# Performance work log

Hardware: AMD Instinct MI355X
Metric: run time of the kernel (lower is better)

The kernel has to match this reference:

```python
import jax, jax.numpy as jnp
import numpy as np

B, S, I, H, E, F, K = 512, 512, 128, 128, 8, 20, 2


def setup_inputs() -> dict:
    key = jax.random.key(0)
    ks = jax.random.split(key, 12)
    u = lambda k, shape, a: jax.random.uniform(k, shape, jnp.float32, -a, a)
    bound_h = 1.0 / np.sqrt(H)
    bound_f = 1.0 / np.sqrt(F)
    return {
        "x": jax.random.normal(ks[0], (B, S, I), jnp.float32),
        "w_gate": jax.random.normal(ks[1], (I, E), jnp.float32),
        "W_ih": u(ks[2], (E, H, I), 0.1),
        "W_hh": u(ks[3], (E, H, H), 0.1),
        "b_ih": u(ks[4], (E, H), bound_h),
        "b_hh": u(ks[5], (E, H), bound_h),
        "fc1_w": u(ks[6], (E, F, H), bound_h),
        "fc1_b": u(ks[7], (E, F), bound_h),
        "fc2_w": u(ks[8], (E, 1, F), bound_f),
        "fc2_b": u(ks[9], (E, 1), bound_f),
    }


def _cv_squared(v):
    v = v.astype(jnp.float32)
    return jnp.var(v, ddof=1) / (jnp.mean(v) ** 2 + 1e-10)


def reference(x, w_gate, W_ih, W_hh, b_ih, b_hh, fc1_w, fc1_b, fc2_w, fc2_b):
    loss_coef = 0.01
    b, s, i = x.shape
    e = w_gate.shape[1]
    # --- top-k gating (noisy_gating=False path) ---
    x_mean = x.mean(axis=1)                       # [B, I]
    logits = x_mean @ w_gate                      # [B, E]
    m = min(K + 1, e)
    top_vals, top_idx = jax.lax.top_k(logits, m)
    topk_gates = jax.nn.softmax(top_vals[:, :K], axis=1)
    gates = jnp.zeros_like(logits).at[jnp.arange(b)[:, None], top_idx[:, :K]].set(topk_gates)
    importance = gates.sum(0)
    load = (gates > 0).sum(0).astype(jnp.float32)
    loss = (_cv_squared(importance) + _cv_squared(load)) * loss_coef
    # --- experts: batched tanh-RNN over all experts (gates zero out unselected) ---
    h0 = jnp.zeros((e, b, W_hh.shape[1]), x.dtype)
    xs = jnp.swapaxes(x, 0, 1)                    # [S, B, I]
    def step(h, xt):
        h = jnp.tanh(jnp.einsum('bi,ehi->ebh', xt, W_ih) + b_ih[:, None, :]
                     + jnp.einsum('ebh,egh->ebg', h, W_hh) + b_hh[:, None, :])
        return h, None
    hT, _ = jax.lax.scan(step, h0, xs)            # [E, B, H] last hidden state
    z = jnp.tanh(jnp.einsum('ebh,efh->ebf', hT, fc1_w) + fc1_b[:, None, :])
    out = jnp.einsum('ebf,eof->ebo', z, fc2_w) + fc2_b[:, None, :]  # [E, B, 1]
    # --- weighted combine: y[b] = sum_e gates[b,e] * expert_e(x[b]) ---
    y = jnp.einsum('be,ebo->bo', gates, out)      # [B, 1]
    return y, loss
```

## Files before the change

### kernel.cpp

```cpp
#include <hip/hip_runtime.h>
#include <math.h>

#define B_SZ 512
#define S_SZ 512
#define E_NUM 8
#define F_DIM 20
#define BM 16
#define MAXBLK 71

typedef __attribute__((ext_vector_type(8))) _Float16 f16x8;
typedef __attribute__((ext_vector_type(4))) float f32x4;
#define MFMAH(a, b, c) __builtin_amdgcn_mfma_f32_16x16x32_f16(a, b, c, 0, 0, 0)

__device__ __forceinline__ unsigned pk16(float a, float b) {
  _Float16 ha = (_Float16)a, hb = (_Float16)b;
  unsigned short ua = __builtin_bit_cast(unsigned short, ha);
  unsigned short ub = __builtin_bit_cast(unsigned short, hb);
  return (unsigned)ua | ((unsigned)ub << 16);
}
__device__ __forceinline__ float ftanh(float x) {
  float e = __expf(x + x);
  float r;
  asm("v_rcp_f32 %0, %1" : "=v"(r) : "v"(e + 1.0f));
  return fmaf(-2.0f, r, 1.0f);
}

#define BAR() do {                                        \
  asm volatile("s_waitcnt lgkmcnt(0)" ::: "memory");      \
  __builtin_amdgcn_s_barrier();                           \
  asm volatile("" ::: "memory");                          \
} while (0)

__global__ __launch_bounds__(256) void k_wsplit16(
    const float* __restrict__ W, _Float16* __restrict__ Wh,
    _Float16* __restrict__ Wl) {
  int idx = (blockIdx.x * 256 + threadIdx.x) * 8;
  float4 a = *(const float4*)(W + idx);
  float4 b = *(const float4*)(W + idx + 4);
  float v[8] = {a.x, a.y, a.z, a.w, b.x, b.y, b.z, b.w};
  f16x8 h, l;
#pragma unroll
  for (int j = 0; j < 8; j++) {
    _Float16 hh = (_Float16)v[j];
    h[j] = hh;
    l[j] = (_Float16)((v[j] - (float)hh) * 1024.0f);
  }
  *(f16x8*)(Wh + idx) = h;
  *(f16x8*)(Wl + idx) = l;
}

__global__ __launch_bounds__(512) void k_mean_logits(
    const float* __restrict__ x, const float* __restrict__ w_gate,
    float* __restrict__ logits) {
  __shared__ float sm[512];
  __shared__ float xm[128];
  int b = blockIdx.x;
  int t = threadIdx.x;
  int i = t & 127, s0 = t >> 7;
  const float* xb = x + (size_t)b * (S_SZ * 128);
  float acc = 0.f;
  for (int s = s0; s < S_SZ; s += 4) acc += xb[s * 128 + i];
  sm[t] = acc;
  __syncthreads();
  if (t < 128)
    xm[t] = (sm[t] + sm[t + 128] + sm[t + 256] + sm[t + 384]) * (1.0f / 512.0f);
  __syncthreads();
  if (t < E_NUM) {
    float acc2 = 0.f;
    for (int ii = 0; ii < 128; ii++) acc2 += xm[ii] * w_gate[ii * E_NUM + t];
    logits[b * E_NUM + t] = acc2;
  }
}

__global__ __launch_bounds__(512) void k_gate(
    const float* __restrict__ logits, float* __restrict__ sel_g,
    int* __restrict__ pair_b, int* __restrict__ pair_of,
    int* __restrict__ blk_e, int* __restrict__ blk_p0,
    int* __restrict__ blk_nr, int* __restrict__ nblk,
    float* __restrict__ loss_out) {
  __shared__ float gmat[512][8];
  __shared__ int cnt[8], base[8], pos[8];
  __shared__ float imps[8];
  int t = threadIdx.x;
  if (t < 8) { cnt[t] = 0; pos[t] = 0; }
  float lv[8];
#pragma unroll
  for (int e = 0; e < 8; e++) {
    lv[e] = logits[t * 8 + e];
    gmat[t][e] = 0.f;
  }
  __syncthreads();
  float v0 = -INFINITY, v1 = -INFINITY;
  int i0 = 0, i1 = 0;
#pragma unroll
  for (int e = 0; e < 8; e++) {
    float v = lv[e];
    if (v > v0) { v1 = v0; i1 = i0; v0 = v; i0 = e; }
    else if (v > v1) { v1 = v; i1 = e; }
  }
  float ex = expf(v1 - v0);
  float inv = 1.0f / (1.0f + ex);
  float g0 = inv, g1 = ex * inv;
  gmat[t][i0] = g0;
  gmat[t][i1] = g1;
  atomicAdd(&cnt[i0], 1);
  atomicAdd(&cnt[i1], 1);
  sel_g[t * 2] = g0;
  sel_g[t * 2 + 1] = g1;
  __syncthreads();
  if (t == 0) {
    int o = 0;
    for (int e = 0; e < 8; e++) { base[e] = o; o += cnt[e]; }
    int nb = 0;
    for (int e = 0; e < 8; e++)
      for (int off = 0; off < cnt[e]; off += BM) {
        blk_e[nb] = e;
        blk_p0[nb] = base[e] + off;
        blk_nr[nb] = min(BM, cnt[e] - off);
        nb++;
      }
    *nblk = nb;
  }
  if (t < 8) {
    float s = 0.f;
    for (int bb = 0; bb < 512; bb++) s += gmat[bb][t];
    imps[t] = s;
  }
  __syncthreads();
  {
    int r = atomicAdd(&pos[i0], 1);
    int p = base[i0] + r;
    pair_b[p] = t;
    pair_of[t * 2] = p;
  }
  {
    int r = atomicAdd(&pos[i1], 1);
    int p = base[i1] + r;
    pair_b[p] = t;
    pair_of[t * 2 + 1] = p;
  }
  if (t == 0) {
    float mi = 0.f, ml = 0.f;
#pragma unroll
    for (int e = 0; e < 8; e++) { mi += imps[e]; ml += (float)cnt[e]; }
    mi *= 0.125f; ml *= 0.125f;
    float vi = 0.f, vl = 0.f;
#pragma unroll
    for (int e = 0; e < 8; e++) {
      float di = imps[e] - mi; vi += di * di;
      float dl = (float)cnt[e] - ml; vl += dl * dl;
    }
    vi *= (1.0f / 7.0f);
    vl *= (1.0f / 7.0f);
    loss_out[0] = 0.01f * (vi / (mi * mi + 1e-10f) + vl / (ml * ml + 1e-10f));
  }
}

__global__ __launch_bounds__(512, 2) void k_moe(
    const float* __restrict__ x, const _Float16* __restrict__ Wih_h,
    const _Float16* __restrict__ Wih_l, const float* __restrict__ W_hh,
    const float* __restrict__ b_ih, const float* __restrict__ b_hh,
    const float* __restrict__ fc1_w, const float* __restrict__ fc1_b,
    const float* __restrict__ fc2_w, const float* __restrict__ fc2_b,
    const int* __restrict__ pair_b, const int* __restrict__ blk_e,
    const int* __restrict__ blk_p0, const int* __restrict__ blk_nr,
    const int* __restrict__ nblk, float* __restrict__ outp) {
  __shared__ unsigned short sX[4][2048];
  __shared__ float sP[2][2048];
  __shared__ unsigned short sH[2][2048];
  __shared__ float sZ[BM * F_DIM];

  int blk = blockIdx.x;
  if (blk >= *nblk) return;
  int e = blk_e[blk], p0 = blk_p0[blk], nr = blk_nr[blk];
  int tid = threadIdx.x;
  int lane = tid & 63, g = lane >> 4, ln = lane & 15;
  int wv = tid >> 6;

  char* sxb = (char*)&sX[0][0];
  char* spb = (char*)&sP[0][0];
  char* shb = (char*)&sH[0][0];

  ((unsigned int*)shb)[tid] = 0;
  ((unsigned int*)shb)[tid + 512] = 0;

  int swz = (ln & 7) << 4;
  int rdoff[4];
#pragma unroll
  for (int ks = 0; ks < 4; ks++) rdoff[ks] = (ln * 256 + ks * 64 + g * 16) ^ swz;

  const f32x4 Z4 = {0.f, 0.f, 0.f, 0.f};

  if (wv < 4) {
    int w = wv;
    f16x8 wih_h[2][4], wih_l[2][4];
#pragma unroll
    for (int m = 0; m < 2; m++) {
      int row = (2 * w + m) * 16 + ln;
      const _Float16* bh = Wih_h + (size_t)e * 16384 + row * 128 + g * 8;
      const _Float16* bl = Wih_l + (size_t)e * 16384 + row * 128 + g * 8;
#pragma unroll
      for (int ks = 0; ks < 4; ks++) {
        wih_h[m][ks] = *(const f16x8*)(bh + ks * 32);
        wih_l[m][ks] = *(const f16x8*)(bl + ks * 32);
      }
    }
    f32x4 biasv[2];
#pragma unroll
    for (int m = 0; m < 2; m++)
#pragma unroll
      for (int r = 0; r < 4; r++) {
        int h = (2 * w + m) * 16 + g * 4 + r;
        biasv[m][r] = b_ih[e * 128 + h] + b_hh[e * 128 + h];
      }
    int pwoff[2];
#pragma unroll
    for (int m = 0; m < 2; m++)
      pwoff[m] = (2 * w + m) * 1024 + g * 256 + ln * 16;

    int srow = 4 * w + (lane >> 4);
    int k0 = (lane & 15) * 8;
    int sb = pair_b[p0 + (srow < nr ? srow : 0)];
    const char* xsrc = (const char*)x + (size_t)sb * (S_SZ * 512) + k0 * 4;
    int stoff = (srow * 256 + k0 * 2) ^ ((srow & 7) << 4);

    float4 xa0, xa1, xb0, xb1;

#define LDX(B0, B1, STEP)                                                    \
  do {                                                                       \
    B0 = *(const float4*)(xsrc + (size_t)(STEP) * 512);                      \
    B1 = *(const float4*)(xsrc + (size_t)(STEP) * 512 + 16);                 \
  } while (0)

#define STG(WS, B0, B1)                                                      \
  do {                                                                       \
    float v[8] = {B0.x, B0.y, B0.z, B0.w, B1.x, B1.y, B1.z, B1.w};           \
    f16x8 hx;                                                                \
    _Pragma("unroll") for (int j = 0; j < 8; j++) hx[j] = (_Float16)v[j];    \
    *(f16x8*)(sxb + ((WS) << 12) + stoff) = hx;                              \
  } while (0)

#define PRD(XS, PS)                                                          \
  do {                                                                       \
    f16x8 Xf[4];                                                             \
    _Pragma("unroll") for (int ks = 0; ks < 4; ks++)                         \
        Xf[ks] = *(const f16x8*)(sxb + ((XS) << 12) + rdoff[ks]);            \
    _Pragma("unroll") for (int m = 0; m < 2; m++) {                          \
      f32x4 pA = biasv[m];                                                   \
      _Pragma("unroll") for (int ks = 0; ks < 4; ks++)                       \
          pA = MFMAH(wih_h[m][ks], Xf[ks], pA);                              \
      f32x4 pB = Z4;                                                         \
      _Pragma("unroll") for (int ks = 0; ks < 4; ks++)                       \
          pB = MFMAH(wih_l[m][ks], Xf[ks], pB);                              \
      _Pragma("unroll") for (int r = 0; r < 4; r++)                          \
          pA[r] = fmaf(pB[r], 0.0009765625f, pA[r]);                         \
      *(f32x4*)(spb + ((PS) << 13) + pwoff[m]) = pA;                         \
    }                                                                        \
  } while (0)

    LDX(xa0, xa1, 0);
    LDX(xb0, xb1, 1);
    STG(0, xa0, xa1);
    STG(1, xb0, xb1);
    LDX(xa0, xa1, 2);
    LDX(xb0, xb1, 3);
    BAR();
    PRD(0, 0);
    STG(2, xa0, xa1);
    LDX(xa0, xa1, 4);
    BAR();

#pragma unroll 1
    for (int r4 = 0; r4 < 504; r4 += 4) {
      PRD(1, 1); STG(3, xb0, xb1); LDX(xb0, xb1, r4 + 5); BAR();
      PRD(2, 0); STG(0, xa0, xa1); LDX(xa0, xa1, r4 + 6); BAR();
      PRD(3, 1); STG(1, xb0, xb1); LDX(xb0, xb1, r4 + 7); BAR();
      PRD(0, 0); STG(2, xa0, xa1); LDX(xa0, xa1, r4 + 8); BAR();
    }
    PRD(1, 1); STG(3, xb0, xb1); LDX(xb0, xb1, 509); BAR();
    PRD(2, 0); STG(0, xa0, xa1); LDX(xa0, xa1, 510); BAR();
    PRD(3, 1); STG(1, xb0, xb1); LDX(xb0, xb1, 511); BAR();
    PRD(0, 0); STG(2, xa0, xa1); BAR();
    PRD(1, 1); STG(3, xb0, xb1); BAR();
    PRD(2, 0); BAR();
    PRD(3, 1); BAR();
    BAR();
#undef PRD
#undef STG
#undef LDX
  } else {
    int w2 = wv - 4;
    f16x8 wh[2][4], wl[2][4];
#pragma unroll
    for (int m = 0; m < 2; m++) {
      int row = (2 * w2 + m) * 16 + ln;
      const float* bh = W_hh + (size_t)e * 16384 + row * 128 + g * 8;
#pragma unroll
      for (int ks = 0; ks < 4; ks++) {
        float4 a = *(const float4*)(bh + ks * 32);
        float4 b = *(const float4*)(bh + ks * 32 + 4);
        float v[8] = {a.x, a.y, a.z, a.w, b.x, b.y, b.z, b.w};
        f16x8 h, l;
#pragma unroll
        for (int j = 0; j < 8; j++) {
          _Float16 hh = (_Float16)v[j];
          h[j] = hh;
          l[j] = (_Float16)((v[j] - (float)hh) * 1024.0f);
        }
        wh[m][ks] = h;
        wl[m][ks] = l;
      }
    }
    int proff[2], wroff[2];
#pragma unroll
    for (int m = 0; m < 2; m++) {
      proff[m] = (2 * w2 + m) * 1024 + g * 256 + ln * 16;
      wroff[m] = (ln * 256 + (2 * w2 + m) * 32 + g * 8) ^ swz;
    }

#define CRD(RS)                                                              \
  do {                                                                       \
    f16x8 Hf[4];                                                             \
    _Pragma("unroll") for (int ks = 0; ks < 4; ks++)                         \
        Hf[ks] = *(const f16x8*)(shb + (RS) * 4096 + rdoff[ks]);             \
    _Pragma("unroll") for (int m = 0; m < 2; m++) {                          \
      f32x4 preA = *(const f32x4*)(spb + ((RS) << 13) + proff[m]);           \
      _Pragma("unroll") for (int ks = 0; ks < 4; ks++)                       \
          preA = MFMAH(wh[m][ks], Hf[ks], preA);                             \
      f32x4 preB = Z4;                                                       \
      _Pragma("unroll") for (int ks = 0; ks < 4; ks++)                       \
          preB = MFMAH(wl[m][ks], Hf[ks], preB);                             \
      _Pragma("unroll") for (int r = 0; r < 4; r++)                          \
          preA[r] = fmaf(preB[r], 0.0009765625f, preA[r]);                   \
      float t0 = ftanh(preA[0]), t1 = ftanh(preA[1]);                        \
      float t2 = ftanh(preA[2]), t3 = ftanh(preA[3]);                        \
      uint2 hv = {pk16(t0, t1), pk16(t2, t3)};                               \
      *(uint2*)(shb + ((RS) ^ 1) * 4096 + wroff[m]) = hv;                    \
    }                                                                        \
  } while (0)

    BAR();
    BAR();
#pragma unroll 1
    for (int it = 0; it < 128; it++) {
      CRD(0); BAR();
      CRD(1); BAR();
      CRD(0); BAR();
      CRD(1); BAR();
    }
#undef CRD
  }

  {
    int p = tid >> 5, q = tid & 31;
    if (q < F_DIM) {
      float acc = fc1_b[e * F_DIM + q];
      const float* w1 = fc1_w + (size_t)e * (F_DIM * 128) + q * 128;
      for (int k = 0; k < 128; k++) {
        int off = (p * 256 + k * 2) ^ ((p & 7) << 4);
        float h = (float)(*(const _Float16*)(shb + off));
        acc = fmaf(h, w1[k], acc);
      }
      sZ[p * F_DIM + q] = ftanh(acc);
    }
  }
  __syncthreads();
  if (tid < BM) {
    float acc = fc2_b[e];
#pragma unroll
    for (int f = 0; f < F_DIM; f++)
      acc += sZ[tid * F_DIM + f] * fc2_w[e * F_DIM + f];
    if (tid < nr) outp[p0 + tid] = acc;
  }
}

__global__ void k_combine(const float* __restrict__ sel_g,
                          const int* __restrict__ pair_of,
                          const float* __restrict__ outp,
                          float* __restrict__ y) {
  int b = blockIdx.x * blockDim.x + threadIdx.x;
  if (b < B_SZ)
    y[b] = sel_g[2 * b] * outp[pair_of[2 * b]] +
           sel_g[2 * b + 1] * outp[pair_of[2 * b + 1]];
}

extern "C" void kernel_launch(void* const* d_in, const int* in_sizes, int n_in,
                              void* d_out, int out_size, void* d_ws,
                              size_t ws_size, hipStream_t stream) {
  (void)in_sizes; (void)n_in; (void)out_size; (void)ws_size;
  const float* x      = (const float*)d_in[0];
  const float* w_gate = (const float*)d_in[1];
  const float* W_ih   = (const float*)d_in[2];
  const float* W_hh   = (const float*)d_in[3];
  const float* b_ih   = (const float*)d_in[4];
  const float* b_hh   = (const float*)d_in[5];
  const float* fc1_w  = (const float*)d_in[6];
  const float* fc1_b  = (const float*)d_in[7];
  const float* fc2_w  = (const float*)d_in[8];
  const float* fc2_b  = (const float*)d_in[9];
  float* out = (float*)d_out;

  float* logits = (float*)d_ws;
  float* sel_g  = logits + 4096;
  int*   pair_b = (int*)(sel_g + 1024);
  int*   pair_of= pair_b + 1024;
  int*   blk_e  = pair_of + 1024;
  int*   blk_p0 = blk_e + 128;
  int*   blk_nr = blk_p0 + 128;
  int*   nblk   = blk_nr + 128;
  float* outp   = (float*)(nblk + 8);
  _Float16* Wih_h = (_Float16*)((char*)d_ws + 65536);
  _Float16* Wih_l = Wih_h + 131072;

  k_wsplit16<<<64, 256, 0, stream>>>(W_ih, Wih_h, Wih_l);
  k_mean_logits<<<B_SZ, 512, 0, stream>>>(x, w_gate, logits);
  k_gate<<<1, 512, 0, stream>>>(logits, sel_g, pair_b, pair_of, blk_e, blk_p0,
                                blk_nr, nblk, out + 512);
  k_moe<<<MAXBLK, 512, 0, stream>>>(x, Wih_h, Wih_l, W_hh, b_ih, b_hh, fc1_w,
                                    fc1_b, fc2_w, fc2_b, pair_b, blk_e,
                                    blk_p0, blk_nr, nblk, outp);
  k_combine<<<2, 256, 0, stream>>>(sel_g, pair_of, outp, out);
}
```

Measured before the change: 346.1 us.

## Deepen input-projection pipeline and split recurrent MFMA chains with prefetch

The producer warps now run two steps ahead of the recurrent warps, writing into a four-slot precomputed-projection buffer instead of two. The recurrent warps prefetch the next step's projection into registers before issuing their MFMAs. Each 4-deep dependent MFMA chain is split into two independent 2-deep chains and summed afterwards, which shortens the serial critical path per timestep. MFMA issue is also raised in priority with s_setprio. This costs extra LDS (sP doubles) and more accumulator registers, which may reduce occupancy.

```diff
diff --git a/kernel.cpp b/kernel.cpp
--- a/kernel.cpp
+++ b/kernel.cpp
@@ -166,7 +166,7 @@
     const int* __restrict__ blk_p0, const int* __restrict__ blk_nr,
     const int* __restrict__ nblk, float* __restrict__ outp) {
   __shared__ unsigned short sX[4][2048];
-  __shared__ float sP[2][2048];
+  __shared__ float sP[4][2048];
   __shared__ unsigned short sH[2][2048];
   __shared__ float sZ[BM * F_DIM];
 
@@ -240,21 +240,26 @@
     *(f16x8*)(sxb + ((WS) << 12) + stoff) = hx;                              \
   } while (0)
 
-#define PRD(XS, PS)                                                          \
+#define PRD(S)                                                               \
   do {                                                                       \
-    f16x8 Xf[4];                                                             \
-    _Pragma("unroll") for (int ks = 0; ks < 4; ks++)                         \
-        Xf[ks] = *(const f16x8*)(sxb + ((XS) << 12) + rdoff[ks]);            \
+    f16x8 Xf0 = *(const f16x8*)(sxb + ((S) << 12) + rdoff[0]);               \
+    f16x8 Xf1 = *(const f16x8*)(sxb + ((S) << 12) + rdoff[1]);               \
+    f16x8 Xf2 = *(const f16x8*)(sxb + ((S) << 12) + rdoff[2]);               \
+    f16x8 Xf3 = *(const f16x8*)(sxb + ((S) << 12) + rdoff[3]);               \
     _Pragma("unroll") for (int m = 0; m < 2; m++) {                          \
       f32x4 pA = biasv[m];                                                   \
-      _Pragma("unroll") for (int ks = 0; ks < 4; ks++)                       \
-          pA = MFMAH(wih_h[m][ks], Xf[ks], pA);                              \
+      pA = MFMAH(wih_h[m][0], Xf0, pA);                                      \
+      pA = MFMAH(wih_h[m][1], Xf1, pA);                                      \
+      pA = MFMAH(wih_h[m][2], Xf2, pA);                                      \
+      pA = MFMAH(wih_h[m][3], Xf3, pA);                                      \
       f32x4 pB = Z4;                                                         \
-      _Pragma("unroll") for (int ks = 0; ks < 4; ks++)                       \
-          pB = MFMAH(wih_l[m][ks], Xf[ks], pB);                              \
+      pB = MFMAH(wih_l[m][0], Xf0, pB);                                      \
+      pB = MFMAH(wih_l[m][1], Xf1, pB);                                      \
+      pB = MFMAH(wih_l[m][2], Xf2, pB);                                      \
+      pB = MFMAH(wih_l[m][3], Xf3, pB);                                      \
       _Pragma("unroll") for (int r = 0; r < 4; r++)                          \
           pA[r] = fmaf(pB[r], 0.0009765625f, pA[r]);                         \
-      *(f32x4*)(spb + ((PS) << 13) + pwoff[m]) = pA;                         \
+      *(f32x4*)(spb + ((S) << 13) + pwoff[m]) = pA;                          \
     }                                                                        \
   } while (0)
 
@@ -263,27 +268,27 @@
     STG(0, xa0, xa1);
     STG(1, xb0, xb1);
     LDX(xa0, xa1, 2);
+    STG(2, xa0, xa1);
     LDX(xb0, xb1, 3);
     BAR();
-    PRD(0, 0);
-    STG(2, xa0, xa1);
-    LDX(xa0, xa1, 4);
+    PRD(0);
+    PRD(1);
     BAR();
 
 #pragma unroll 1
     for (int r4 = 0; r4 < 504; r4 += 4) {
-      PRD(1, 1); STG(3, xb0, xb1); LDX(xb0, xb1, r4 + 5); BAR();
-      PRD(2, 0); STG(0, xa0, xa1); LDX(xa0, xa1, r4 + 6); BAR();
-      PRD(3, 1); STG(1, xb0, xb1); LDX(xb0, xb1, r4 + 7); BAR();
-      PRD(0, 0); STG(2, xa0, xa1); LDX(xa0, xa1, r4 + 8); BAR();
-    }
-    PRD(1, 1); STG(3, xb0, xb1); LDX(xb0, xb1, 509); BAR();
-    PRD(2, 0); STG(0, xa0, xa1); LDX(xa0, xa1, 510); BAR();
-    PRD(3, 1); STG(1, xb0, xb1); LDX(xb0, xb1, 511); BAR();
-    PRD(0, 0); STG(2, xa0, xa1); BAR();
-    PRD(1, 1); STG(3, xb0, xb1); BAR();
-    PRD(2, 0); BAR();
-    PRD(3, 1); BAR();
+      PRD(2); STG(3, xb0, xb1); LDX(xa0, xa1, r4 + 4); BAR();
+      PRD(3); STG(0, xa0, xa1); LDX(xb0, xb1, r4 + 5); BAR();
+      PRD(0); STG(1, xb0, xb1); LDX(xa0, xa1, r4 + 6); BAR();
+      PRD(1); STG(2, xa0, xa1); LDX(xb0, xb1, r4 + 7); BAR();
+    }
+    PRD(2); STG(3, xb0, xb1); LDX(xa0, xa1, 508); BAR();
+    PRD(3); STG(0, xa0, xa1); LDX(xb0, xb1, 509); BAR();
+    PRD(0); STG(1, xb0, xb1); LDX(xa0, xa1, 510); BAR();
+    PRD(1); STG(2, xa0, xa1); LDX(xb0, xb1, 511); BAR();
+    PRD(2); STG(3, xb0, xb1); BAR();
+    PRD(3); BAR();
+    BAR();
     BAR();
 #undef PRD
 #undef STG
@@ -318,35 +323,55 @@
       wroff[m] = (ln * 256 + (2 * w2 + m) * 32 + g * 8) ^ swz;
     }
 
-#define CRD(RS)                                                              \
+#define CRD(RS, PSN, PU0, PU1, PN0, PN1)                                     \
   do {                                                                       \
-    f16x8 Hf[4];                                                             \
-    _Pragma("unroll") for (int ks = 0; ks < 4; ks++)                         \
-        Hf[ks] = *(const f16x8*)(shb + (RS) * 4096 + rdoff[ks]);             \
-    _Pragma("unroll") for (int m = 0; m < 2; m++) {                          \
-      f32x4 preA = *(const f32x4*)(spb + ((RS) << 13) + proff[m]);           \
-      _Pragma("unroll") for (int ks = 0; ks < 4; ks++)                       \
-          preA = MFMAH(wh[m][ks], Hf[ks], preA);                             \
-      f32x4 preB = Z4;                                                       \
-      _Pragma("unroll") for (int ks = 0; ks < 4; ks++)                       \
-          preB = MFMAH(wl[m][ks], Hf[ks], preB);                             \
-      _Pragma("unroll") for (int r = 0; r < 4; r++)                          \
-          preA[r] = fmaf(preB[r], 0.0009765625f, preA[r]);                   \
-      float t0 = ftanh(preA[0]), t1 = ftanh(preA[1]);                        \
-      float t2 = ftanh(preA[2]), t3 = ftanh(preA[3]);                        \
+    f16x8 Hf0 = *(const f16x8*)(shb + (RS)*4096 + rdoff[0]);                 \
+    f16x8 Hf1 = *(const f16x8*)(shb + (RS)*4096 + rdoff[1]);                 \
+    f16x8 Hf2 = *(const f16x8*)(shb + (RS)*4096 + rdoff[2]);                 \
+    f16x8 Hf3 = *(const f16x8*)(shb + (RS)*4096 + rdoff[3]);                 \
+    PN0 = *(const f32x4*)(spb + ((PSN) << 13) + proff[0]);                   \
+    PN1 = *(const f32x4*)(spb + ((PSN) << 13) + proff[1]);                   \
+    __builtin_amdgcn_s_setprio(1);                                           \
+    f32x4 a0 = MFMAH(wh[0][0], Hf0, PU0); a0 = MFMAH(wh[0][1], Hf1, a0);     \
+    f32x4 b0 = MFMAH(wh[0][2], Hf2, Z4);  b0 = MFMAH(wh[0][3], Hf3, b0);     \
+    f32x4 c0 = MFMAH(wl[0][0], Hf0, Z4);  c0 = MFMAH(wl[0][1], Hf1, c0);     \
+    f32x4 d0 = MFMAH(wl[0][2], Hf2, Z4);  d0 = MFMAH(wl[0][3], Hf3, d0);     \
+    f32x4 a1 = MFMAH(wh[1][0], Hf0, PU1); a1 = MFMAH(wh[1][1], Hf1, a1);     \
+    f32x4 b1 = MFMAH(wh[1][2], Hf2, Z4);  b1 = MFMAH(wh[1][3], Hf3, b1);     \
+    f32x4 c1 = MFMAH(wl[1][0], Hf0, Z4);  c1 = MFMAH(wl[1][1], Hf1, c1);     \
+    f32x4 d1 = MFMAH(wl[1][2], Hf2, Z4);  d1 = MFMAH(wl[1][3], Hf3, d1);     \
+    __builtin_amdgcn_s_setprio(0);                                           \
+    f32x4 pre0, pre1;                                                        \
+    _Pragma("unroll") for (int r = 0; r < 4; r++) {                          \
+      pre0[r] = (a0[r] + b0[r]) + (c0[r] + d0[r]) * 0.0009765625f;           \
+      pre1[r] = (a1[r] + b1[r]) + (c1[r] + d1[r]) * 0.0009765625f;           \
+    }                                                                        \
+    {                                                                        \
+      float t0 = ftanh(pre0[0]), t1 = ftanh(pre0[1]);                        \
+      float t2 = ftanh(pre0[2]), t3 = ftanh(pre0[3]);                        \
       uint2 hv = {pk16(t0, t1), pk16(t2, t3)};                               \
-      *(uint2*)(shb + ((RS) ^ 1) * 4096 + wroff[m]) = hv;                    \
+      *(uint2*)(shb + ((RS) ^ 1) * 4096 + wroff[0]) = hv;                    \
     }                                                                        \
+    {                                                                        \
+      float t0 = ftanh(pre1[0]), t1 = ftanh(pre1[1]);                        \
+      float t2 = ftanh(pre1[2]), t3 = ftanh(pre1[3]);                        \
+      uint2 hv = {pk16(t0, t1), pk16(t2, t3)};                               \
+      *(uint2*)(shb + ((RS) ^ 1) * 4096 + wroff[1]) = hv;                    \
+    }                                                                        \
+    BAR();                                                                   \
   } while (0)
 
-    BAR();
-    BAR();
+    f32x4 prA0, prA1, prB0, prB1;
+    BAR();
+    BAR();
+    prA0 = *(const f32x4*)(spb + proff[0]);
+    prA1 = *(const f32x4*)(spb + proff[1]);
 #pragma unroll 1
     for (int it = 0; it < 128; it++) {
-      CRD(0); BAR();
-      CRD(1); BAR();
-      CRD(0); BAR();
-      CRD(1); BAR();
+      CRD(0, 1, prA0, prA1, prB0, prB1);
+      CRD(1, 2, prB0, prB1, prA0, prA1);
+      CRD(0, 3, prA0, prA1, prB0, prB1);
+      CRD(1, 0, prB0, prB1, prA0, prA1);
     }
 #undef CRD
   }
```

New measurement: 425.9 us, median of 2. 1.23x slower.
